# Kernel optimization log

Hardware: AMD Instinct MI355X
Metric: run time of the kernel (lower is better)

## Reference

```python
import jax, jax.numpy as jnp
import numpy as np

C_S, C_Z, C_ATOM, H, RBF = 128, 64, 16, 4, 16
N_RES, E_RES, N_ATOM, E_ATOM = 1000, 4000, 14000, 784000


def _p(key, shape, scale=0.05):
    return (jax.random.normal(key, shape, dtype=jnp.float32) * scale)


def setup_inputs() -> dict:
    key = jax.random.key(0)
    ks = jax.random.split(key, 24)
    inp = {
        "node_features": jax.random.normal(ks[0], (N_RES, C_S), dtype=jnp.float32),
        "res_edge_features": jax.random.normal(ks[1], (E_RES, C_Z), dtype=jnp.float32),
        "res_edge_index": jax.random.randint(ks[2], (2, E_RES), 0, N_RES),
        "atom_features": jax.random.normal(ks[3], (N_ATOM, C_ATOM), dtype=jnp.float32),
        "atom_coords": jax.random.normal(ks[4], (N_ATOM, 3), dtype=jnp.float32),
        "cross_atom_edge_index": jax.random.randint(ks[5], (2, E_ATOM), 0, N_ATOM),
        "atom_edge_to_res_edge": jax.random.randint(ks[6], (E_ATOM,), 0, E_RES),
        # atom_dist_embed MLP: RBF -> RBF -> RBF -> H
        "rbf_w1": _p(ks[7], (RBF, RBF)), "rbf_b1": jnp.zeros((RBF,), jnp.float32),
        "rbf_w2": _p(ks[8], (RBF, RBF)), "rbf_b2": jnp.zeros((RBF,), jnp.float32),
        "rbf_w3": _p(ks[9], (RBF, H)),  "rbf_b3": jnp.zeros((H,), jnp.float32),
        # res_level_bias MLP: (2*c_s + c_z) -> c_atom -> H
        "rb_w1": _p(ks[10], (2 * C_S + C_Z, C_ATOM)), "rb_b1": jnp.zeros((C_ATOM,), jnp.float32),
        "rb_w2": _p(ks[11], (C_ATOM, H)), "rb_b2": jnp.zeros((H,), jnp.float32),
        # q / kv / out projections
        "wq": _p(ks[12], (C_ATOM, C_ATOM * H)),     "bq": jnp.zeros((C_ATOM * H,), jnp.float32),
        "wkv": _p(ks[13], (C_ATOM, 2 * C_ATOM * H)), "bkv": jnp.zeros((2 * C_ATOM * H,), jnp.float32),
        "wo": _p(ks[14], (C_ATOM * H, C_ATOM)),     "bo": jnp.zeros((C_ATOM,), jnp.float32),
    }
    return inp


def _rbf(d, d_min=0.0, d_max=20.0, d_count=RBF):
    mu = jnp.linspace(d_min, d_max, d_count, dtype=jnp.float32)
    sigma = (d_max - d_min) / d_count
    return jnp.exp(-(((d[..., None] - mu) / sigma) ** 2))


def _seg_softmax(x, idx, n_seg):
    # scatter-softmax over segments (pyg_utils.softmax), per head column
    m = jax.ops.segment_max(x, idx, num_segments=n_seg)
    e = jnp.exp(x - m[idx])
    s = jax.ops.segment_sum(e, idx, num_segments=n_seg)
    return e / (s[idx] + 1e-16)


def reference(node_features, res_edge_features, res_edge_index, atom_features,
              atom_coords, cross_atom_edge_index, atom_edge_to_res_edge,
              rbf_w1, rbf_b1, rbf_w2, rbf_b2, rbf_w3, rbf_b3,
              rb_w1, rb_b1, rb_w2, rb_b2, wq, bq, wkv, bkv, wo, bo,
              eps=1e-8):
    src = cross_atom_edge_index[1]
    dst = cross_atom_edge_index[0]

    # RBF distance bias  [E_atom, H]
    vec = atom_coords[dst] - atom_coords[src]
    d = jnp.linalg.norm(vec + eps, axis=-1)
    h = jax.nn.relu(_rbf(d) @ rbf_w1 + rbf_b1)
    h = jax.nn.relu(h @ rbf_w2 + rbf_b2)
    atom_dist_bias = h @ rbf_w3 + rbf_b3

    # residue-level bias  [E_res, H]
    cat = jnp.concatenate([res_edge_features,
                           node_features[res_edge_index[0]],
                           node_features[res_edge_index[1]]], axis=-1)
    res_level_bias = jax.nn.relu(cat @ rb_w1 + rb_b1) @ rb_w2 + rb_b2

    # gathered q / k / v  [E_atom, H, c_atom]
    q = (atom_features @ wq + bq)[src].reshape(-1, H, C_ATOM)
    kv = (atom_features @ wkv + bkv)[dst].reshape(-1, H, 2 * C_ATOM)
    k, v = kv[..., :C_ATOM], kv[..., C_ATOM:]

    R = jnp.einsum('ehc,ehc->eh', q, k) / np.sqrt(C_ATOM)
    R = R + res_level_bias[atom_edge_to_res_edge] + atom_dist_bias

    # atom-level scatter-softmax over edges grouped by src atom
    alpha = _seg_softmax(R, src, N_ATOM)

    # residue-level: scatter-mean of scores per residue edge, then softmax by dst res
    cnt = jax.ops.segment_sum(jnp.ones((R.shape[0],), R.dtype),
                              atom_edge_to_res_edge, num_segments=E_RES)
    block_r = jax.ops.segment_sum(R, atom_edge_to_res_edge, num_segments=E_RES)
    block_r = block_r / jnp.clip(cnt, 1.0)[:, None]
    beta = _seg_softmax(block_r, res_edge_index[1], N_RES)

    w = alpha * beta[atom_edge_to_res_edge]           # [E_atom, H]
    atom_update = jax.ops.segment_sum(w[..., None] * v, src, num_segments=N_ATOM)
    return atom_update.reshape(-1, H * C_ATOM) @ wo + bo
```

## Files before the change

kernel.cpp:

```cpp
#include <hip/hip_runtime.h>

#define NH 4
#define N_RES 1000
#define E_RES 4000
#define N_ATOM 14000
#define E_ATOM 784000
#define MAXS 128
#define NBRE 256
#define TABN 16385
#define TINV 512.0f
#define NHB 256
#define EPB 3063

#define HIST_BLKS NHB
#define PROJ_BLKS ((N_ATOM * 192 + 255) / 256)
#define RLB_BLKS (E_RES / 4)
#define TAB_BLKS ((TABN + 255) / 256)

typedef float f32x4 __attribute__((ext_vector_type(4)));

__device__ __forceinline__ unsigned enc_f(float f) {
  unsigned u = __float_as_uint(f);
  return (u & 0x80000000u) ? ~u : (u | 0x80000000u);
}
__device__ __forceinline__ float dec_f(unsigned e) {
  unsigned u = (e & 0x80000000u) ? (e & 0x7FFFFFFFu) : ~e;
  return __uint_as_float(u);
}

__global__ __launch_bounds__(256) void kA(
    const int* __restrict__ cei, int* __restrict__ ghist,
    const float* __restrict__ af, const float* __restrict__ wq,
    const float* __restrict__ bq, const float* __restrict__ wkv,
    const float* __restrict__ bkv, float* __restrict__ Qa,
    float* __restrict__ Ka, float* __restrict__ Va,
    const float* __restrict__ ref_, const float* __restrict__ nf,
    const int* __restrict__ rei, const float* __restrict__ w1,
    const float* __restrict__ b1, const float* __restrict__ w2,
    const float* __restrict__ b2, float* __restrict__ rlb,
    const float* __restrict__ rw1, const float* __restrict__ rb1,
    const float* __restrict__ rw2, const float* __restrict__ rb2,
    const float* __restrict__ rw3, const float* __restrict__ rb3,
    f32x4* __restrict__ tab) {
  __shared__ unsigned lhist[N_ATOM / 2];
  int b = blockIdx.x;
  if (b < HIST_BLKS) {
    int t = threadIdx.x;
    for (int j = t; j < N_ATOM / 2; j += 256) lhist[j] = 0u;
    __syncthreads();
    int e0 = b * EPB;
    int e1 = e0 + EPB;
    if (e1 > E_ATOM) e1 = E_ATOM;
    for (int e = e0 + t; e < e1; e += 256) {
      int src = cei[E_ATOM + e];
      atomicAdd(&lhist[src >> 1], (src & 1) ? 65536u : 1u);
    }
    __syncthreads();
    int2* gh = (int2*)(ghist + (size_t)b * N_ATOM);
    for (int j = t; j < N_ATOM / 2; j += 256) {
      unsigned v = lhist[j];
      gh[j] = make_int2((int)(v & 0xFFFFu), (int)(v >> 16));
    }
  } else if (b < HIST_BLKS + PROJ_BLKS) {
    int tid = (b - HIST_BLKS) * 256 + threadIdx.x;
    if (tid < N_ATOM * 192) {
      int a = tid / 192, j = tid % 192;
      const float* row = af + a * 16;
      if (j < 64) {
        float acc = bq[j];
#pragma unroll
        for (int i = 0; i < 16; ++i) acc += row[i] * wq[i * 64 + j];
        Qa[a * 64 + j] = acc;
      } else if (j < 128) {
        int jj = j - 64;
        int col = ((jj >> 4) << 5) + (jj & 15);
        float acc = bkv[col];
#pragma unroll
        for (int i = 0; i < 16; ++i) acc += row[i] * wkv[i * 128 + col];
        Ka[a * 64 + jj] = acc;
      } else {
        int jj = j - 128;
        int col = ((jj >> 4) << 5) + 16 + (jj & 15);
        float acc = bkv[col];
#pragma unroll
        for (int i = 0; i < 16; ++i) acc += row[i] * wkv[i * 128 + col];
        Va[a * 64 + jj] = acc;
      }
    }
  } else if (b < HIST_BLKS + PROJ_BLKS + RLB_BLKS) {
    __shared__ float hid[4][16];
    int sub = threadIdx.x >> 6, l = threadIdx.x & 63;
    int r = (b - HIST_BLKS - PROJ_BLKS) * 4 + sub;
    int r0 = rei[r], r1 = rei[E_RES + r];
    int j = l >> 2, pq = l & 3;
    float acc = 0.f;
    for (int i = pq; i < 320; i += 4) {
      float cc;
      if (i < 64) cc = ref_[r * 64 + i];
      else if (i < 192) cc = nf[r0 * 128 + (i - 64)];
      else cc = nf[r1 * 128 + (i - 192)];
      acc += cc * w1[i * 16 + j];
    }
    acc += __shfl_xor(acc, 1);
    acc += __shfl_xor(acc, 2);
    if (pq == 0) hid[sub][j] = fmaxf(acc + b1[j], 0.f);
    __syncthreads();
    if (l < 4) {
      float o = b2[l];
#pragma unroll
      for (int jj = 0; jj < 16; ++jj) o += hid[sub][jj] * w2[jj * 4 + l];
      rlb[r * 4 + l] = o;
    }
  } else {
    int i = (b - HIST_BLKS - PROJ_BLKS - RLB_BLKS) * 256 + threadIdx.x;
    if (i < TABN) {
      float d = (float)i * (1.0f / TINV);
      float rb[16], h1[16], h2[16];
      const float step = 20.0f / 15.0f;
      const float inv_sigma = 1.0f / 1.25f;
#pragma unroll
      for (int jj = 0; jj < 16; ++jj) {
        float t = (d - jj * step) * inv_sigma;
        rb[jj] = __expf(-t * t);
      }
#pragma unroll
      for (int k = 0; k < 16; ++k) {
        float acc = rb1[k];
#pragma unroll
        for (int jj = 0; jj < 16; ++jj) acc += rb[jj] * rw1[jj * 16 + k];
        h1[k] = fmaxf(acc, 0.f);
      }
#pragma unroll
      for (int k = 0; k < 16; ++k) {
        float acc = rb2[k];
#pragma unroll
        for (int jj = 0; jj < 16; ++jj) acc += h1[jj] * rw2[jj * 16 + k];
        h2[k] = fmaxf(acc, 0.f);
      }
      f32x4 o;
#pragma unroll
      for (int h = 0; h < NH; ++h) {
        float acc = rb3[h];
#pragma unroll
        for (int jj = 0; jj < 16; ++jj) acc += h2[jj] * rw3[jj * 4 + h];
        o[h] = acc;
      }
      tab[i] = o;
    }
  }
}

__global__ __launch_bounds__(256) void k_ofs(const int* __restrict__ ghist,
                                             int* __restrict__ ofs,
                                             int* __restrict__ cnt_src) {
  int s = blockIdx.x * blockDim.x + threadIdx.x;
  if (s >= N_ATOM) return;
  int run = 0;
  for (int b = 0; b < NHB; ++b) {
    int v = ghist[(size_t)b * N_ATOM + s];
    ofs[(size_t)b * N_ATOM + s] = run;
    run += v;
  }
  cnt_src[s] = (run > MAXS) ? MAXS : run;
}

__global__ __launch_bounds__(256) void k_scat(
    const int* __restrict__ cei, const int* __restrict__ aer,
    const int* __restrict__ ofs, unsigned* __restrict__ pay) {
  __shared__ int lbase[N_ATOM];
  int b = blockIdx.x, t = threadIdx.x;
  const int* orow = ofs + (size_t)b * N_ATOM;
  for (int j = t; j < N_ATOM; j += 256) lbase[j] = orow[j];
  __syncthreads();
  int e0 = b * EPB;
  int e1 = e0 + EPB;
  if (e1 > E_ATOM) e1 = E_ATOM;
  for (int e = e0 + t; e < e1; e += 256) {
    int src = cei[E_ATOM + e];
    int dst = cei[e];
    int re = aer[e];
    int slot = atomicAdd(&lbase[src], 1);
    if (slot < MAXS)
      pay[(size_t)src * MAXS + slot] = (unsigned)dst | ((unsigned)re << 16);
  }
}

__global__ __launch_bounds__(256) void k_edgeR(
    const int* __restrict__ cnt_src, const unsigned* __restrict__ pay,
    const float* __restrict__ coords, const float* __restrict__ Qa,
    const float* __restrict__ Ka, const float* __restrict__ rlb,
    const f32x4* __restrict__ tab, float* __restrict__ R_slab,
    f32x4* __restrict__ msm, f32x4* __restrict__ mss) {
  int l = threadIdx.x & 63;
  int a = blockIdx.x * 4 + (threadIdx.x >> 6);
  int n = cnt_src[a];
  if (n > MAXS) n = MAXS;
  size_t base = (size_t)a * MAXS;
  float ax = coords[a * 3 + 0], ay = coords[a * 3 + 1], az = coords[a * 3 + 2];
  const float4* qp = (const float4*)(Qa + (size_t)a * 64);
  bool a0 = l < n, a1 = l + 64 < n;
  f32x4 R0, R1;
#pragma unroll
  for (int sl = 0; sl < 2; ++sl) {
    bool act = sl ? a1 : a0;
    f32x4 Rv = {-3.0e38f, -3.0e38f, -3.0e38f, -3.0e38f};
    if (act) {
      int s = l + sl * 64;
      unsigned pr = pay[base + s];
      int dst = (int)(pr & 0xFFFFu);
      int re = (int)(pr >> 16);
      float vx = coords[dst * 3 + 0] - ax + 1e-8f;
      float vy = coords[dst * 3 + 1] - ay + 1e-8f;
      float vz = coords[dst * 3 + 2] - az + 1e-8f;
      float d = sqrtf(vx * vx + vy * vy + vz * vz);
      float x = d * TINV;
      int i = (int)x;
      if (i > TABN - 2) i = TABN - 2;
      float fr = x - (float)i;
      f32x4 t0 = tab[i], t1 = tab[i + 1];
      f32x4 adb = t0 + (t1 - t0) * fr;
      const float4* kp = (const float4*)(Ka + (size_t)dst * 64);
      float4 rlb4 = *(const float4*)(rlb + re * 4);
      const float* rlbp = (const float*)&rlb4;
#pragma unroll
      for (int h = 0; h < NH; ++h) {
        float dot = 0.f;
#pragma unroll
        for (int v4 = 0; v4 < 4; ++v4) {
          float4 q4 = qp[h * 4 + v4];
          float4 k4 = kp[h * 4 + v4];
          dot += q4.x * k4.x + q4.y * k4.y + q4.z * k4.z + q4.w * k4.w;
        }
        Rv[h] = dot * 0.25f + rlbp[h] + adb[h];
      }
      __builtin_nontemporal_store(Rv, (f32x4*)(R_slab + (base + s) * 4));
    }
    if (sl) R1 = Rv; else R0 = Rv;
  }
  f32x4 mx;
#pragma unroll
  for (int h = 0; h < NH; ++h) mx[h] = fmaxf(R0[h], R1[h]);
#pragma unroll
  for (int off = 1; off < 64; off <<= 1) {
#pragma unroll
    for (int h = 0; h < NH; ++h) mx[h] = fmaxf(mx[h], __shfl_xor(mx[h], off));
  }
  f32x4 ex;
#pragma unroll
  for (int h = 0; h < NH; ++h)
    ex[h] = (a0 ? __expf(R0[h] - mx[h]) : 0.f) +
            (a1 ? __expf(R1[h] - mx[h]) : 0.f);
#pragma unroll
  for (int off = 1; off < 64; off <<= 1) {
#pragma unroll
    for (int h = 0; h < NH; ++h) ex[h] += __shfl_xor(ex[h], off);
  }
  if (l == 0) {
    msm[a] = mx;
    mss[a] = ex;
  }
}

__global__ __launch_bounds__(1024) void k_re2(
    const int* __restrict__ cnt_src, const unsigned* __restrict__ pay,
    const float* __restrict__ R_slab, int* __restrict__ cntg,
    float* __restrict__ br_g) {
  __shared__ __align__(16) unsigned char smraw[64000];
  int* scnt = (int*)smraw;
  float* sbr = (float*)smraw;
  int tid = threadIdx.x;
  int bid = blockIdx.x;
  int wv = tid >> 6, lane = tid & 63;
  int gw = bid * 16 + wv;
  for (int j = tid; j < E_RES; j += 1024) scnt[j] = 0;
  __syncthreads();
  for (int a = gw; a < N_ATOM; a += NBRE * 16) {
    int n = cnt_src[a];
    if (n > MAXS) n = MAXS;
    size_t base = (size_t)a * MAXS;
    for (int i = lane; i < n; i += 64) {
      int re = (int)(pay[base + i] >> 16);
      atomicAdd(&scnt[re], 1);
    }
  }
  __syncthreads();
  for (int j = tid; j < E_RES; j += 1024) cntg[bid * E_RES + j] = scnt[j];
  __syncthreads();
  for (int j = tid; j < E_RES * 4; j += 1024) sbr[j] = 0.f;
  __syncthreads();
  for (int a = gw; a < N_ATOM; a += NBRE * 16) {
    int n = cnt_src[a];
    if (n > MAXS) n = MAXS;
    size_t base = (size_t)a * MAXS;
    for (int i = lane; i < n; i += 64) {
      int re = (int)(pay[base + i] >> 16);
      f32x4 r = *(const f32x4*)(R_slab + (base + i) * 4);
      atomicAdd(&sbr[re * 4 + 0], r[0]);
      atomicAdd(&sbr[re * 4 + 1], r[1]);
      atomicAdd(&sbr[re * 4 + 2], r[2]);
      atomicAdd(&sbr[re * 4 + 3], r[3]);
    }
  }
  __syncthreads();
  for (int j = tid; j < E_RES * 4; j += 1024)
    br_g[(size_t)bid * E_RES * 4 + j] = sbr[j];
}

__global__ __launch_bounds__(256) void k_red(const float* __restrict__ br_g,
                                             const int* __restrict__ cntg,
                                             float* __restrict__ block_r) {
  int t = blockIdx.x * blockDim.x + threadIdx.x;
  if (t >= E_RES * 4) return;
  int r = t >> 2;
  float s = 0.f;
  int c = 0;
  for (int b = 0; b < NBRE; ++b) {
    s += br_g[(size_t)b * E_RES * 4 + t];
    c += cntg[b * E_RES + r];
  }
  block_r[t] = s / fmaxf((float)c, 1.0f);
}

__global__ __launch_bounds__(1024) void k_br23(
    const float* __restrict__ block_r, const int* __restrict__ rei,
    float* __restrict__ beta) {
  __shared__ unsigned resm[N_RES * 4];
  __shared__ float ress[N_RES * 4];
  int tid = threadIdx.x;
  for (int j = tid; j < N_RES * 4; j += 1024) { resm[j] = 0u; ress[j] = 0.f; }
  __syncthreads();
  float brv[4][4];
  int r1v[4];
  for (int k = 0; k < 4; ++k) {
    int r = tid + k * 1024;
    if (r < E_RES) {
      r1v[k] = rei[E_RES + r];
#pragma unroll
      for (int h = 0; h < 4; ++h) {
        brv[k][h] = block_r[r * 4 + h];
        atomicMax(&resm[r1v[k] * 4 + h], enc_f(brv[k][h]));
      }
    }
  }
  __syncthreads();
  for (int k = 0; k < 4; ++k) {
    int r = tid + k * 1024;
    if (r < E_RES) {
#pragma unroll
      for (int h = 0; h < 4; ++h)
        atomicAdd(&ress[r1v[k] * 4 + h],
                  __expf(brv[k][h] - dec_f(resm[r1v[k] * 4 + h])));
    }
  }
  __syncthreads();
  for (int k = 0; k < 4; ++k) {
    int r = tid + k * 1024;
    if (r < E_RES) {
#pragma unroll
      for (int h = 0; h < 4; ++h)
        beta[r * 4 + h] = __expf(brv[k][h] - dec_f(resm[r1v[k] * 4 + h])) /
                          (ress[r1v[k] * 4 + h] + 1e-16f);
    }
  }
}

__global__ __launch_bounds__(256) void k_src(
    const int* __restrict__ cnt_src, const unsigned* __restrict__ pay,
    const float* __restrict__ R_slab, const float* __restrict__ beta,
    const float* __restrict__ Va, const f32x4* __restrict__ msm,
    const f32x4* __restrict__ mss, const float* __restrict__ wo,
    const float* __restrict__ bo, float* __restrict__ out) {
  __shared__ float sau[4][64];
  int wv = threadIdx.x >> 6, l = threadIdx.x & 63;
  int wid = blockIdx.x * 4 + wv;
  int n = cnt_src[wid];
  if (n > MAXS) n = MAXS;
  int h = l >> 4;
  size_t rbase = (size_t)wid * MAXS;
  f32x4 m4 = msm[wid], s4 = mss[wid];
  float mh = m4[h];
  float sden = s4[h] + 1e-16f;
  float acc = 0.f;
#pragma unroll 2
  for (int i = 0; i < n; ++i) {
    unsigned pr = pay[rbase + i];
    int dst = (int)(pr & 0xFFFFu);
    int re = (int)(pr >> 16);
    float rv = R_slab[(rbase + i) * 4 + h];
    float bt = beta[re * 4 + h];
    float v = Va[(size_t)dst * 64 + l];
    acc += __expf(rv - mh) * bt * v;
  }
  sau[wv][l] = acc / sden;
  __syncthreads();
  int p = l >> 4, c = l & 15;
  float part = 0.f;
#pragma unroll
  for (int jj = 0; jj < 16; ++jj)
    part += sau[wv][p * 16 + jj] * wo[(p * 16 + jj) * 16 + c];
  part += __shfl_down(part, 32);
  part += __shfl_down(part, 16);
  if (l < 16) out[wid * 16 + c] = part + bo[c];
}

extern "C" void kernel_launch(void* const* d_in, const int* in_sizes, int n_in,
                              void* d_out, int out_size, void* d_ws,
                              size_t ws_size, hipStream_t stream) {
  const float* nf   = (const float*)d_in[0];
  const float* ref_ = (const float*)d_in[1];
  const int*   rei  = (const int*)d_in[2];
  const float* af   = (const float*)d_in[3];
  const float* co   = (const float*)d_in[4];
  const int*   cei  = (const int*)d_in[5];
  const int*   aer  = (const int*)d_in[6];
  const float* rw1  = (const float*)d_in[7];
  const float* rb1  = (const float*)d_in[8];
  const float* rw2  = (const float*)d_in[9];
  const float* rb2  = (const float*)d_in[10];
  const float* rw3  = (const float*)d_in[11];
  const float* rb3  = (const float*)d_in[12];
  const float* w1   = (const float*)d_in[13];
  const float* b1   = (const float*)d_in[14];
  const float* w2   = (const float*)d_in[15];
  const float* b2   = (const float*)d_in[16];
  const float* wq   = (const float*)d_in[17];
  const float* bq   = (const float*)d_in[18];
  const float* wkv  = (const float*)d_in[19];
  const float* bkv  = (const float*)d_in[20];
  const float* wo   = (const float*)d_in[21];
  const float* bo   = (const float*)d_in[22];
  float* out = (float*)d_out;

  float* ws = (float*)d_ws;
  float*    Qa      = ws;
  float*    Ka      = Qa + 896000;
  float*    Va      = Ka + 896000;
  float*    rlb     = Va + 896000;
  float*    R_slab  = rlb + 16000;
  unsigned* pay     = (unsigned*)(R_slab + 7168000);
  float*    br_g    = (float*)(pay + 1792000);
  int*      cntg    = (int*)(br_g + 4096000);
  int*      cnt_src = cntg + 1024000;
  float*    block_r = (float*)(cnt_src + 14000);
  f32x4*    tab     = (f32x4*)(block_r + 16000);
  f32x4*    msm     = (f32x4*)((float*)tab + 65544);
  f32x4*    mss     = (f32x4*)((float*)msm + 56000);
  int*      ghist   = (int*)br_g;
  int*      ofs     = (int*)R_slab;
  float*    beta    = Ka + 16000;

  kA<<<HIST_BLKS + PROJ_BLKS + RLB_BLKS + TAB_BLKS, 256, 0, stream>>>(
      cei, ghist, af, wq, bq, wkv, bkv, Qa, Ka, Va, ref_, nf, rei, w1, b1, w2,
      b2, rlb, rw1, rb1, rw2, rb2, rw3, rb3, tab);
  k_ofs<<<(N_ATOM + 255) / 256, 256, 0, stream>>>(ghist, ofs, cnt_src);
  k_scat<<<NHB, 256, 0, stream>>>(cei, aer, ofs, pay);
  k_edgeR<<<N_ATOM / 4, 256, 0, stream>>>(cnt_src, pay, co, Qa, Ka, rlb, tab,
                                          R_slab, msm, mss);
  k_re2<<<NBRE, 1024, 0, stream>>>(cnt_src, pay, R_slab, cntg, br_g);
  k_red<<<(E_RES * 4 + 255) / 256, 256, 0, stream>>>(br_g, cntg, block_r);
  k_br23<<<1, 1024, 0, stream>>>(block_r, rei, beta);
  k_src<<<N_ATOM / 4, 256, 0, stream>>>(cnt_src, pay, R_slab, beta, Va, msm,
                                        mss, wo, bo, out);
}
```

Baseline: 247.6 us.

## Pack histogram, offsets and residue counts as 16-bit to cut intermediate traffic

Splits the histogram out of the fused prologue kernel into its own launch. The per-block histograms, prefix offsets and residue-edge counts are stored packed as 16-bit values instead of 32-bit ints, which roughly halves the global traffic through these large per-block intermediate arrays. k_re2 now does one pass over the payload, updating counts and score sums together instead of two passes. k_src's unroll is raised to 4. The risks are 16-bit overflow if per-block counts ever exceed 65535, and the smem layout change in k_re2 (about 72KB now) may lower occupancy.

```diff
diff --git a/kernel.cpp b/kernel.cpp
--- a/kernel.cpp
+++ b/kernel.cpp
@@ -12,7 +12,6 @@
 #define NHB 256
 #define EPB 3063
 
-#define HIST_BLKS NHB
 #define PROJ_BLKS ((N_ATOM * 192 + 255) / 256)
 #define RLB_BLKS (E_RES / 4)
 #define TAB_BLKS ((TABN + 255) / 256)
@@ -28,8 +27,24 @@
   return __uint_as_float(u);
 }
 
-__global__ __launch_bounds__(256) void kA(
-    const int* __restrict__ cei, int* __restrict__ ghist,
+__global__ __launch_bounds__(256) void k_hist(const int* __restrict__ cei,
+                                              unsigned* __restrict__ ghistP) {
+  __shared__ unsigned lhist[N_ATOM / 2];
+  int b = blockIdx.x, t = threadIdx.x;
+  for (int j = t; j < N_ATOM / 2; j += 256) lhist[j] = 0u;
+  __syncthreads();
+  int e0 = b * EPB, e1 = e0 + EPB;
+  if (e1 > E_ATOM) e1 = E_ATOM;
+  for (int e = e0 + t; e < e1; e += 256) {
+    int src = cei[E_ATOM + e];
+    atomicAdd(&lhist[src >> 1], (src & 1) ? 65536u : 1u);
+  }
+  __syncthreads();
+  unsigned* gh = ghistP + (size_t)b * (N_ATOM / 2);
+  for (int j = t; j < N_ATOM / 2; j += 256) gh[j] = lhist[j];
+}
+
+__global__ __launch_bounds__(256) void kA2(
     const float* __restrict__ af, const float* __restrict__ wq,
     const float* __restrict__ bq, const float* __restrict__ wkv,
     const float* __restrict__ bkv, float* __restrict__ Qa,
@@ -42,27 +57,10 @@
     const float* __restrict__ rw2, const float* __restrict__ rb2,
     const float* __restrict__ rw3, const float* __restrict__ rb3,
     f32x4* __restrict__ tab) {
-  __shared__ unsigned lhist[N_ATOM / 2];
+  __shared__ float hid[4][16];
   int b = blockIdx.x;
-  if (b < HIST_BLKS) {
-    int t = threadIdx.x;
-    for (int j = t; j < N_ATOM / 2; j += 256) lhist[j] = 0u;
-    __syncthreads();
-    int e0 = b * EPB;
-    int e1 = e0 + EPB;
-    if (e1 > E_ATOM) e1 = E_ATOM;
-    for (int e = e0 + t; e < e1; e += 256) {
-      int src = cei[E_ATOM + e];
-      atomicAdd(&lhist[src >> 1], (src & 1) ? 65536u : 1u);
-    }
-    __syncthreads();
-    int2* gh = (int2*)(ghist + (size_t)b * N_ATOM);
-    for (int j = t; j < N_ATOM / 2; j += 256) {
-      unsigned v = lhist[j];
-      gh[j] = make_int2((int)(v & 0xFFFFu), (int)(v >> 16));
-    }
-  } else if (b < HIST_BLKS + PROJ_BLKS) {
-    int tid = (b - HIST_BLKS) * 256 + threadIdx.x;
+  if (b < PROJ_BLKS) {
+    int tid = b * 256 + threadIdx.x;
     if (tid < N_ATOM * 192) {
       int a = tid / 192, j = tid % 192;
       const float* row = af + a * 16;
@@ -87,10 +85,9 @@
         Va[a * 64 + jj] = acc;
       }
     }
-  } else if (b < HIST_BLKS + PROJ_BLKS + RLB_BLKS) {
-    __shared__ float hid[4][16];
+  } else if (b < PROJ_BLKS + RLB_BLKS) {
     int sub = threadIdx.x >> 6, l = threadIdx.x & 63;
-    int r = (b - HIST_BLKS - PROJ_BLKS) * 4 + sub;
+    int r = (b - PROJ_BLKS) * 4 + sub;
     int r0 = rei[r], r1 = rei[E_RES + r];
     int j = l >> 2, pq = l & 3;
     float acc = 0.f;
@@ -112,7 +109,7 @@
       rlb[r * 4 + l] = o;
     }
   } else {
-    int i = (b - HIST_BLKS - PROJ_BLKS - RLB_BLKS) * 256 + threadIdx.x;
+    int i = (b - PROJ_BLKS - RLB_BLKS) * 256 + threadIdx.x;
     if (i < TABN) {
       float d = (float)i * (1.0f / TINV);
       float rb[16], h1[16], h2[16];
@@ -150,15 +147,18 @@
   }
 }
 
-__global__ __launch_bounds__(256) void k_ofs(const int* __restrict__ ghist,
-                                             int* __restrict__ ofs,
+__global__ __launch_bounds__(256) void k_ofs(const unsigned* __restrict__ ghistP,
+                                             unsigned short* __restrict__ ofs16,
                                              int* __restrict__ cnt_src) {
   int s = blockIdx.x * blockDim.x + threadIdx.x;
   if (s >= N_ATOM) return;
+  int half = s >> 1;
+  unsigned sel = (s & 1) ? 16 : 0;
   int run = 0;
+#pragma unroll 8
   for (int b = 0; b < NHB; ++b) {
-    int v = ghist[(size_t)b * N_ATOM + s];
-    ofs[(size_t)b * N_ATOM + s] = run;
+    int v = (int)((ghistP[(size_t)b * (N_ATOM / 2) + half] >> sel) & 0xFFFFu);
+    ofs16[(size_t)b * N_ATOM + s] = (unsigned short)run;
     run += v;
   }
   cnt_src[s] = (run > MAXS) ? MAXS : run;
@@ -166,14 +166,17 @@
 
 __global__ __launch_bounds__(256) void k_scat(
     const int* __restrict__ cei, const int* __restrict__ aer,
-    const int* __restrict__ ofs, unsigned* __restrict__ pay) {
+    const unsigned* __restrict__ ofs16P, unsigned* __restrict__ pay) {
   __shared__ int lbase[N_ATOM];
   int b = blockIdx.x, t = threadIdx.x;
-  const int* orow = ofs + (size_t)b * N_ATOM;
-  for (int j = t; j < N_ATOM; j += 256) lbase[j] = orow[j];
-  __syncthreads();
-  int e0 = b * EPB;
-  int e1 = e0 + EPB;
+  const unsigned* orow = ofs16P + (size_t)b * (N_ATOM / 2);
+  for (int j = t; j < N_ATOM / 2; j += 256) {
+    unsigned v = orow[j];
+    lbase[2 * j] = (int)(v & 0xFFFFu);
+    lbase[2 * j + 1] = (int)(v >> 16);
+  }
+  __syncthreads();
+  int e0 = b * EPB, e1 = e0 + EPB;
   if (e1 > E_ATOM) e1 = E_ATOM;
   for (int e = e0 + t; e < e1; e += 256) {
     int src = cei[E_ATOM + e];
@@ -263,16 +266,16 @@
 
 __global__ __launch_bounds__(1024) void k_re2(
     const int* __restrict__ cnt_src, const unsigned* __restrict__ pay,
-    const float* __restrict__ R_slab, int* __restrict__ cntg,
+    const float* __restrict__ R_slab, unsigned short* __restrict__ cntg16,
     float* __restrict__ br_g) {
-  __shared__ __align__(16) unsigned char smraw[64000];
-  int* scnt = (int*)smraw;
-  float* sbr = (float*)smraw;
+  __shared__ unsigned scntP[E_RES / 2];
+  __shared__ float sbr[E_RES * 4];
   int tid = threadIdx.x;
   int bid = blockIdx.x;
   int wv = tid >> 6, lane = tid & 63;
   int gw = bid * 16 + wv;
-  for (int j = tid; j < E_RES; j += 1024) scnt[j] = 0;
+  for (int j = tid; j < E_RES / 2; j += 1024) scntP[j] = 0u;
+  for (int j = tid; j < E_RES * 4; j += 1024) sbr[j] = 0.f;
   __syncthreads();
   for (int a = gw; a < N_ATOM; a += NBRE * 16) {
     int n = cnt_src[a];
@@ -280,20 +283,7 @@
     size_t base = (size_t)a * MAXS;
     for (int i = lane; i < n; i += 64) {
       int re = (int)(pay[base + i] >> 16);
-      atomicAdd(&scnt[re], 1);
-    }
-  }
-  __syncthreads();
-  for (int j = tid; j < E_RES; j += 1024) cntg[bid * E_RES + j] = scnt[j];
-  __syncthreads();
-  for (int j = tid; j < E_RES * 4; j += 1024) sbr[j] = 0.f;
-  __syncthreads();
-  for (int a = gw; a < N_ATOM; a += NBRE * 16) {
-    int n = cnt_src[a];
-    if (n > MAXS) n = MAXS;
-    size_t base = (size_t)a * MAXS;
-    for (int i = lane; i < n; i += 64) {
-      int re = (int)(pay[base + i] >> 16);
+      atomicAdd(&scntP[re >> 1], (re & 1) ? 65536u : 1u);
       f32x4 r = *(const f32x4*)(R_slab + (base + i) * 4);
       atomicAdd(&sbr[re * 4 + 0], r[0]);
       atomicAdd(&sbr[re * 4 + 1], r[1]);
@@ -302,13 +292,18 @@
     }
   }
   __syncthreads();
+  for (int j = tid; j < E_RES; j += 1024) {
+    unsigned v = scntP[j >> 1];
+    cntg16[(size_t)bid * E_RES + j] =
+        (unsigned short)((j & 1) ? (v >> 16) : (v & 0xFFFFu));
+  }
   for (int j = tid; j < E_RES * 4; j += 1024)
     br_g[(size_t)bid * E_RES * 4 + j] = sbr[j];
 }
 
-__global__ __launch_bounds__(256) void k_red(const float* __restrict__ br_g,
-                                             const int* __restrict__ cntg,
-                                             float* __restrict__ block_r) {
+__global__ __launch_bounds__(256) void k_red(
+    const float* __restrict__ br_g, const unsigned short* __restrict__ cntg16,
+    float* __restrict__ block_r) {
   int t = blockIdx.x * blockDim.x + threadIdx.x;
   if (t >= E_RES * 4) return;
   int r = t >> 2;
@@ -316,7 +311,7 @@
   int c = 0;
   for (int b = 0; b < NBRE; ++b) {
     s += br_g[(size_t)b * E_RES * 4 + t];
-    c += cntg[b * E_RES + r];
+    c += (int)cntg16[(size_t)b * E_RES + r];
   }
   block_r[t] = s / fmaxf((float)c, 1.0f);
 }
@@ -381,7 +376,7 @@
   float mh = m4[h];
   float sden = s4[h] + 1e-16f;
   float acc = 0.f;
-#pragma unroll 2
+#pragma unroll 4
   for (int i = 0; i < n; ++i) {
     unsigned pr = pay[rbase + i];
     int dst = (int)(pr & 0xFFFFu);
@@ -439,25 +434,26 @@
   float*    R_slab  = rlb + 16000;
   unsigned* pay     = (unsigned*)(R_slab + 7168000);
   float*    br_g    = (float*)(pay + 1792000);
-  int*      cntg    = (int*)(br_g + 4096000);
-  int*      cnt_src = cntg + 1024000;
+  unsigned short* cntg16 = (unsigned short*)(br_g + 4096000);
+  int*      cnt_src = (int*)(cntg16 + 1024000);
   float*    block_r = (float*)(cnt_src + 14000);
   f32x4*    tab     = (f32x4*)(block_r + 16000);
   f32x4*    msm     = (f32x4*)((float*)tab + 65544);
   f32x4*    mss     = (f32x4*)((float*)msm + 56000);
-  int*      ghist   = (int*)br_g;
-  int*      ofs     = (int*)R_slab;
+  unsigned* ghistP  = (unsigned*)br_g;
+  unsigned short* ofs16 = (unsigned short*)R_slab;
   float*    beta    = Ka + 16000;
 
-  kA<<<HIST_BLKS + PROJ_BLKS + RLB_BLKS + TAB_BLKS, 256, 0, stream>>>(
-      cei, ghist, af, wq, bq, wkv, bkv, Qa, Ka, Va, ref_, nf, rei, w1, b1, w2,
-      b2, rlb, rw1, rb1, rw2, rb2, rw3, rb3, tab);
-  k_ofs<<<(N_ATOM + 255) / 256, 256, 0, stream>>>(ghist, ofs, cnt_src);
-  k_scat<<<NHB, 256, 0, stream>>>(cei, aer, ofs, pay);
+  k_hist<<<NHB, 256, 0, stream>>>(cei, ghistP);
+  kA2<<<PROJ_BLKS + RLB_BLKS + TAB_BLKS, 256, 0, stream>>>(
+      af, wq, bq, wkv, bkv, Qa, Ka, Va, ref_, nf, rei, w1, b1, w2, b2, rlb,
+      rw1, rb1, rw2, rb2, rw3, rb3, tab);
+  k_ofs<<<(N_ATOM + 255) / 256, 256, 0, stream>>>(ghistP, ofs16, cnt_src);
+  k_scat<<<NHB, 256, 0, stream>>>(cei, aer, (const unsigned*)ofs16, pay);
   k_edgeR<<<N_ATOM / 4, 256, 0, stream>>>(cnt_src, pay, co, Qa, Ka, rlb, tab,
                                           R_slab, msm, mss);
-  k_re2<<<NBRE, 1024, 0, stream>>>(cnt_src, pay, R_slab, cntg, br_g);
-  k_red<<<(E_RES * 4 + 255) / 256, 256, 0, stream>>>(br_g, cntg, block_r);
+  k_re2<<<NBRE, 1024, 0, stream>>>(cnt_src, pay, R_slab, cntg16, br_g);
+  k_red<<<(E_RES * 4 + 255) / 256, 256, 0, stream>>>(br_g, cntg16, block_r);
   k_br23<<<1, 1024, 0, stream>>>(block_r, rei, beta);
   k_src<<<N_ATOM / 4, 256, 0, stream>>>(cnt_src, pay, R_slab, beta, Va, msm,
                                         mss, wo, bo, out);
```

New measurement: 237.5 us. 4.1% less time.
